# Performance work log

Hardware: AMD Instinct MI355X
Metric: run time of the kernel (lower is better)

Reference implementation:

```python
import jax, jax.numpy as jnp
import numpy as np

B, N, C, H = 1, 4096, 768, 12
HD = C // H  # 64
EPS = 1e-5


def _rope_freqs(n, hd, theta=10000.0):
    inv = 1.0 / (theta ** (np.arange(0, hd, 2, dtype=np.float32) / hd))  # (hd/2,)
    ang = np.outer(np.arange(n, dtype=np.float32), inv)  # (N, hd/2)
    return jnp.asarray(np.cos(ang)), jnp.asarray(np.sin(ang))


def setup_inputs() -> dict:
    key = jax.random.key(0)
    ks = jax.random.split(key, 5)
    cos, sin = _rope_freqs(N, HD)
    s = lambda d: 1.0 / np.sqrt(d)
    return {
        "x": jax.random.normal(ks[0], (B, N, C), jnp.float32),
        "freqs_cos": cos,
        "freqs_sin": sin,
        "w_qkv": jax.random.normal(ks[1], (3 * C, C), jnp.float32) * s(C),
        "w_proj": jax.random.normal(ks[2], (C, C), jnp.float32) * s(C),
        "b_proj": jnp.zeros((C,), jnp.float32),
        "g1": jnp.ones((C,), jnp.float32),
        "beta1": jnp.zeros((C,), jnp.float32),
        "g2": jnp.ones((C,), jnp.float32),
        "beta2": jnp.zeros((C,), jnp.float32),
        "w_fc1": jax.random.normal(ks[3], (4 * C, C), jnp.float32) * s(C),
        "b_fc1": jnp.zeros((4 * C,), jnp.float32),
        "w_fc2": jax.random.normal(ks[4], (C, 4 * C), jnp.float32) * s(4 * C),
        "b_fc2": jnp.zeros((C,), jnp.float32),
    }


def _layernorm(x, g, b):
    mu = jnp.mean(x, -1, keepdims=True)
    var = jnp.mean(jnp.square(x - mu), -1, keepdims=True)
    return (x - mu) * jax.lax.rsqrt(var + EPS) * g + b


def _apply_rope(t, cos, sin):
    # t: (B, N, H, HD); cos/sin: (N, HD/2) -> broadcast (1, N, 1, HD/2)
    t = t.reshape(*t.shape[:-1], HD // 2, 2)
    t0, t1 = t[..., 0], t[..., 1]
    c = cos[None, :, None, :]
    s = sin[None, :, None, :]
    out = jnp.stack([t0 * c - t1 * s, t0 * s + t1 * c], axis=-1)
    return out.reshape(*out.shape[:-2], HD)


def reference(x, freqs_cos, freqs_sin, w_qkv, w_proj, b_proj, g1, beta1, g2, beta2,
              w_fc1, b_fc1, w_fc2, b_fc2):
    # --- attention branch ---
    h = _layernorm(x, g1, beta1)
    qkv = (h @ w_qkv.T).reshape(B, N, 3, H, HD)
    q, k, v = qkv[:, :, 0], qkv[:, :, 1], qkv[:, :, 2]  # (B,N,H,HD)
    q = _apply_rope(q, freqs_cos, freqs_sin)
    k = _apply_rope(k, freqs_cos, freqs_sin)
    scale = HD ** (-0.5)
    attn = jnp.einsum('bnhd,bmhd->bhnm', q, k) * scale
    attn = jax.nn.softmax(attn, axis=-1)
    o = jnp.einsum('bhnm,bmhd->bnhd', attn, v).reshape(B, N, C)
    x = x + o @ w_proj.T + b_proj
    # --- mlp branch ---
    h = _layernorm(x, g2, beta2)
    h = jax.nn.gelu(h @ w_fc1.T + b_fc1, approximate=False)
    x = x + h @ w_fc2.T + b_fc2
    return x
```

## Files before the change

### kernel.cpp

```cpp
#include <hip/hip_runtime.h>
#include <hip/hip_bf16.h>
#include <math.h>

#define LOG2E 1.44269504088896340736f

typedef short bf16x8 __attribute__((ext_vector_type(8)));
typedef float f32x4 __attribute__((ext_vector_type(4)));

static __device__ __forceinline__ float bf2f(ushort u){
  union { float f; unsigned int u; } x; x.u = ((unsigned int)u) << 16; return x.f;
}
static __device__ __forceinline__ ushort f2bf(float f){
  union { float f; unsigned int u; } x; x.f = f;
  unsigned int r = x.u + 0x7fffu + ((x.u >> 16) & 1u);
  return (ushort)(r >> 16);
}
static __device__ __forceinline__ unsigned cvt_pk_bf16(float a, float b){
  unsigned r;
  asm("v_cvt_pk_bf16_f32 %0, %1, %2" : "=v"(r) : "v"(a), "v"(b));
  return r;
}
static __device__ __forceinline__ float fmax3(float a, float b, float c){
  return fmaxf(fmaxf(a, b), c);
}
static __device__ __forceinline__ void gload_lds16(const void* g, void* l){
  __builtin_amdgcn_global_load_lds(
      (const __attribute__((address_space(1))) unsigned int*)g,
      (__attribute__((address_space(3))) unsigned int*)l, 16, 0, 0);
}

__global__ __launch_bounds__(256) void cvt_f32_bf16(const float* __restrict__ src,
                                                    ushort* __restrict__ dst, int n4){
  int i = blockIdx.x * 256 + threadIdx.x;
  if (i < n4){
    float4 v = ((const float4*)src)[i];
    ushort4 o;
    o.x = f2bf(v.x); o.y = f2bf(v.y); o.z = f2bf(v.z); o.w = f2bf(v.w);
    ((ushort4*)dst)[i] = o;
  }
}

__device__ __forceinline__ float block_sum256(float s, float* red){
  #pragma unroll
  for (int off = 32; off; off >>= 1) s += __shfl_xor(s, off, 64);
  int w = threadIdx.x >> 6;
  if ((threadIdx.x & 63) == 0) red[w] = s;
  __syncthreads();
  float tot = red[0] + red[1] + red[2] + red[3];
  __syncthreads();
  return tot;
}

__global__ __launch_bounds__(256) void ln_kernel(const float* __restrict__ x,
                                                 const float* __restrict__ g,
                                                 const float* __restrict__ bta,
                                                 ushort* __restrict__ out){
  __shared__ float red[4];
  int row = blockIdx.x, t = threadIdx.x;
  const float* xr = x + (size_t)row * 768;
  float v0 = xr[t], v1 = xr[t + 256], v2 = xr[t + 512];
  float mu = block_sum256(v0 + v1 + v2, red) * (1.0f / 768.0f);
  float d0 = v0 - mu, d1 = v1 - mu, d2 = v2 - mu;
  float var = block_sum256(d0*d0 + d1*d1 + d2*d2, red) * (1.0f / 768.0f);
  float rs = rsqrtf(var + 1e-5f);
  ushort* orow = out + (size_t)row * 768;
  orow[t]       = f2bf(d0 * rs * g[t]       + bta[t]);
  orow[t + 256] = f2bf(d1 * rs * g[t + 256] + bta[t + 256]);
  orow[t + 512] = f2bf(d2 * rs * g[t + 512] + bta[t + 512]);
}

template<int MODE>
__global__ __launch_bounds__(256) void gemm_bf16(const ushort* __restrict__ A, int lda,
                                                 const ushort* __restrict__ Bm, int ldb,
                                                 int K,
                                                 const float* __restrict__ bias,
                                                 const float* __restrict__ res, int ldr,
                                                 void* __restrict__ out, int ldo){
  __shared__ __align__(16) ushort As[128 * 64];
  __shared__ __align__(16) ushort Bs[128 * 64];
  const int tid = threadIdx.x;
  const int m0 = blockIdx.x * 128, n0 = blockIdx.y * 128;
  const int w = tid >> 6, l = tid & 63;
  const int wm = (w >> 1) * 64, wn = (w & 1) * 64;
  const int lr = l & 15, lg = l >> 4;
  const int lane8 = l >> 3, sl = l & 7;
  const int koff = (MODE == 3) ? blockIdx.z * K : 0;

  f32x4 acc[4][4] = {};

  for (int k0 = 0; k0 < K; k0 += 64){
    #pragma unroll
    for (int j = 0; j < 4; ++j){
      int instr = w * 4 + j;
      int row = instr * 8 + lane8;
      gload_lds16((const char*)A + ((size_t)(m0 + row) * lda + koff + k0) * 2 + ((sl ^ (row & 7)) << 4),
                  (char*)As + instr * 1024);
      gload_lds16((const char*)Bm + ((size_t)(n0 + row) * ldb + koff + k0) * 2 + ((sl ^ (row & 7)) << 4),
                  (char*)Bs + instr * 1024);
    }
    __syncthreads();
    #pragma unroll
    for (int kk = 0; kk < 2; ++kk){
      bf16x8 af[4], bfr[4];
      #pragma unroll
      for (int mi = 0; mi < 4; ++mi){
        int row = wm + mi * 16 + lr;
        int cg = (kk * 4 + lg) ^ (row & 7);
        af[mi] = *(const bf16x8*)(As + row * 64 + cg * 8);
      }
      #pragma unroll
      for (int nj = 0; nj < 4; ++nj){
        int row = wn + nj * 16 + lr;
        int cg = (kk * 4 + lg) ^ (row & 7);
        bfr[nj] = *(const bf16x8*)(Bs + row * 64 + cg * 8);
      }
      #pragma unroll
      for (int mi = 0; mi < 4; ++mi)
        #pragma unroll
        for (int nj = 0; nj < 4; ++nj)
          acc[mi][nj] = __builtin_amdgcn_mfma_f32_16x16x32_bf16(af[mi], bfr[nj], acc[mi][nj], 0, 0, 0);
    }
    __syncthreads();
  }

  const size_t zout = (MODE == 3) ? (size_t)blockIdx.z * gridDim.x * 128 * ldo : 0;

  #pragma unroll
  for (int mi = 0; mi < 4; ++mi){
    #pragma unroll
    for (int nj = 0; nj < 4; ++nj){
      #pragma unroll
      for (int r = 0; r < 4; ++r){
        int grow = m0 + wm + mi * 16 + lg * 4 + r;
        int gcol = n0 + wn + nj * 16 + lr;
        float v = acc[mi][nj][r];
        if (MODE == 0){
          ((ushort*)out)[(size_t)grow * ldo + gcol] = f2bf(v);
        } else if (MODE == 1){
          v += bias[gcol] + res[(size_t)grow * ldr + gcol];
          ((float*)out)[(size_t)grow * ldo + gcol] = v;
        } else if (MODE == 2){
          v += bias[gcol];
          v = 0.5f * v * (1.0f + erff(v * 0.70710678118654752f));
          ((ushort*)out)[(size_t)grow * ldo + gcol] = f2bf(v);
        } else {
          ((float*)out)[zout + (size_t)grow * ldo + gcol] = v;
        }
      }
    }
  }
}

__global__ __launch_bounds__(192) void gemm_combine4(const float* __restrict__ parts,
                                                     const float* __restrict__ bias,
                                                     const float* __restrict__ res,
                                                     float* __restrict__ out){
  int q = blockIdx.x, t = threadIdx.x;
  size_t idx = (size_t)q * 768 + t * 4;
  const size_t seg = (size_t)4096 * 768;
  f32x4 o = *(const f32x4*)(parts + idx);
  #pragma unroll
  for (int s = 1; s < 4; ++s) o += *(const f32x4*)(parts + s * seg + idx);
  f32x4 b = *(const f32x4*)(bias + t * 4);
  f32x4 rr = *(const f32x4*)(res + idx);
  o += b + rr;
  *(f32x4*)(out + idx) = o;
}

__global__ __launch_bounds__(384) void rope_kernel(const ushort* __restrict__ qkv,
                                                   const float* __restrict__ fc,
                                                   const float* __restrict__ fs,
                                                   ushort* __restrict__ Qs,
                                                   ushort* __restrict__ Ks,
                                                   ushort* __restrict__ Vt){
  int n = blockIdx.x, t = threadIdx.x;
  int h = t >> 5, p = t & 31;
  float c = fc[(size_t)n * 32 + p], s = fs[(size_t)n * 32 + p];
  const ushort* row = qkv + (size_t)n * 2304;
  const float qscale = 0.125f * LOG2E;
  {
    float t0 = bf2f(row[h * 64 + 2 * p]), t1 = bf2f(row[h * 64 + 2 * p + 1]);
    ushort* dst = Qs + ((size_t)h * 4096 + n) * 64;
    dst[2 * p]     = f2bf((t0 * c - t1 * s) * qscale);
    dst[2 * p + 1] = f2bf((t0 * s + t1 * c) * qscale);
  }
  {
    float t0 = bf2f(row[768 + h * 64 + 2 * p]), t1 = bf2f(row[768 + h * 64 + 2 * p + 1]);
    ushort* dst = Ks + ((size_t)h * 4096 + n) * 64;
    dst[2 * p]     = f2bf(t0 * c - t1 * s);
    dst[2 * p + 1] = f2bf(t0 * s + t1 * c);
  }
  #pragma unroll
  for (int i = 0; i < 2; ++i){
    int idx = t + i * 384;
    int hh = idx >> 6, d = idx & 63;
    Vt[((size_t)hh * 64 + d) * 4096 + n] = row[1536 + idx];
  }
}

__global__ __launch_bounds__(256) void flash_attn(const ushort* __restrict__ Qs,
                                                  const ushort* __restrict__ Ks,
                                                  const ushort* __restrict__ Vt,
                                                  float* __restrict__ Opart,
                                                  float* __restrict__ Ml){
  __shared__ __align__(16) char smem[32768];
  const int h = blockIdx.y, kh = blockIdx.z;
  const int w = threadIdx.x >> 6, l = threadIdx.x & 63;
  const int lr = l & 15, lg = l >> 4;
  const int lane8 = l >> 3, sl = l & 7;
  const int q0 = blockIdx.x * 128 + w * 32;
  const ushort* Qh = Qs + (size_t)h * (4096 * 64);
  const char* Kh = (const char*)(Ks + (size_t)h * (4096 * 64));
  const char* Vh = (const char*)(Vt + (size_t)h * (64 * 4096));

  bf16x8 qa[2][2];
  #pragma unroll
  for (int qf = 0; qf < 2; ++qf)
    #pragma unroll
    for (int kk = 0; kk < 2; ++kk)
      qa[qf][kk] = *(const bf16x8*)(Qh + (size_t)(q0 + qf * 16 + lr) * 64 + kk * 32 + lg * 8);

  const char* kbase = Kh + (size_t)(kh * 1024 + w * 16 + lane8) * 128;
  const char* vbase = Vh + (size_t)(w * 16 + lane8) * 8192 + kh * 2048 + ((sl ^ lane8) << 4);
  int koff[2];
  #pragma unroll
  for (int j = 0; j < 2; ++j)
    koff[j] = j * 1024 + ((sl ^ ((lane8 & 3) | (((w * 2 + j) & 1) << 2))) << 4);

  const int a_ = lr >> 2, b_ = lr & 3;
  const int krow = 8 * a_ + b_;
  const int f_ = b_ | ((a_ & 1) << 2);
  const int kslot0 = (lg ^ f_) << 4;
  const int kslot1 = ((4 + lg) ^ f_) << 4;
  const int vslot0 = lr * 128 + ((lg ^ (lr & 7)) << 4);
  const int vslot1 = lr * 128 + (((4 + lg) ^ (lr & 7)) << 4);

  f32x4 oacc[2][4] = {};
  f32x4 lacc[2] = {};
  float m_prev[2] = {-1e30f, -1e30f};
  union { unsigned u[4]; bf16x8 v; } ones;
  #pragma unroll
  for (int i = 0; i < 4; ++i) ones.u[i] = 0x3F803F80u;

  auto stage = [&](int tile, char* Kb, char* Vb){
    #pragma unroll
    for (int j = 0; j < 2; ++j){
      gload_lds16(kbase + (size_t)tile * 8192 + koff[j], Kb + (w * 2 + j) * 1024);
      gload_lds16(vbase + (size_t)j * 65536 + (size_t)tile * 128, Vb + (w * 2 + j) * 1024);
    }
  };

  auto compute = [&](const char* Kb, const char* Vb){
    f32x4 s[2][4] = {};
    #pragma unroll
    for (int t = 0; t < 4; ++t){
      const char* kr = Kb + (krow + 4 * (t & 1) + 32 * (t >> 1)) * 128;
      bf16x8 k0 = *(const bf16x8*)(kr + kslot0);
      bf16x8 k1 = *(const bf16x8*)(kr + kslot1);
      #pragma unroll
      for (int qf = 0; qf < 2; ++qf){
        s[qf][t] = __builtin_amdgcn_mfma_f32_16x16x32_bf16(k0, qa[qf][0], s[qf][t], 0, 0, 0);
        s[qf][t] = __builtin_amdgcn_mfma_f32_16x16x32_bf16(k1, qa[qf][1], s[qf][t], 0, 0, 0);
      }
    }
    float mn[2];
    bool defer = true;
    #pragma unroll
    for (int qf = 0; qf < 2; ++qf){
      float m1 = fmax3(s[qf][0][0], s[qf][0][1], s[qf][0][2]);
      float m2 = fmax3(s[qf][0][3], s[qf][1][0], s[qf][1][1]);
      float m3 = fmax3(s[qf][1][2], s[qf][1][3], s[qf][2][0]);
      float m4 = fmax3(s[qf][2][1], s[qf][2][2], s[qf][2][3]);
      float m5 = fmax3(s[qf][3][0], s[qf][3][1], s[qf][3][2]);
      float mb = fmaxf(fmax3(m1, m2, m3), fmax3(m4, m5, s[qf][3][3]));
      mb = fmaxf(mb, __shfl_xor(mb, 16, 64));
      mb = fmaxf(mb, __shfl_xor(mb, 32, 64));
      bool d = (mb - m_prev[qf]) <= 8.0f;
      mn[qf] = d ? m_prev[qf] : mb;
      defer = defer && d;
    }
    if (!__all(defer)){
      #pragma unroll
      for (int qf = 0; qf < 2; ++qf){
        float sc = exp2f(m_prev[qf] - mn[qf]);
        #pragma unroll
        for (int db = 0; db < 4; ++db)
          #pragma unroll
          for (int r = 0; r < 4; ++r) oacc[qf][db][r] *= sc;
        #pragma unroll
        for (int r = 0; r < 4; ++r) lacc[qf][r] *= sc;
        m_prev[qf] = mn[qf];
      }
    }
    #pragma unroll
    for (int qf = 0; qf < 2; ++qf)
      #pragma unroll
      for (int t = 0; t < 4; ++t)
        #pragma unroll
        for (int r = 0; r < 4; ++r)
          s[qf][t][r] = exp2f(s[qf][t][r] - mn[qf]);
    #pragma unroll
    for (int kk = 0; kk < 2; ++kk){
      union { unsigned u[4]; bf16x8 v; } pf[2];
      #pragma unroll
      for (int qf = 0; qf < 2; ++qf){
        pf[qf].u[0] = cvt_pk_bf16(s[qf][2*kk][0],   s[qf][2*kk][1]);
        pf[qf].u[1] = cvt_pk_bf16(s[qf][2*kk][2],   s[qf][2*kk][3]);
        pf[qf].u[2] = cvt_pk_bf16(s[qf][2*kk+1][0], s[qf][2*kk+1][1]);
        pf[qf].u[3] = cvt_pk_bf16(s[qf][2*kk+1][2], s[qf][2*kk+1][3]);
      }
      const int vs = kk ? vslot1 : vslot0;
      #pragma unroll
      for (int db = 0; db < 4; ++db){
        bf16x8 vf = *(const bf16x8*)(Vb + vs + db * 2048);
        #pragma unroll
        for (int qf = 0; qf < 2; ++qf)
          oacc[qf][db] = __builtin_amdgcn_mfma_f32_16x16x32_bf16(vf, pf[qf].v, oacc[qf][db], 0, 0, 0);
      }
      #pragma unroll
      for (int qf = 0; qf < 2; ++qf)
        lacc[qf] = __builtin_amdgcn_mfma_f32_16x16x32_bf16(ones.v, pf[qf].v, lacc[qf], 0, 0, 0);
    }
  };

  char* K0 = smem;          char* V0 = smem + 8192;
  char* K1 = smem + 16384;  char* V1 = smem + 24576;

  stage(0, K0, V0);
  __syncthreads();
  #pragma unroll 1
  for (int it2 = 0; it2 < 8; ++it2){
    stage(2 * it2 + 1, K1, V1);
    compute(K0, V0);
    __syncthreads();
    if (it2 < 7) stage(2 * it2 + 2, K0, V0);
    compute(K1, V1);
    __syncthreads();
  }

  #pragma unroll
  for (int qf = 0; qf < 2; ++qf){
    int q = q0 + qf * 16 + lr;
    float* Op = Opart + ((size_t)(kh * 12 + h) * 4096 + q) * 64;
    #pragma unroll
    for (int db = 0; db < 4; ++db)
      *(f32x4*)(Op + db * 16 + 4 * lg) = oacc[qf][db];
    if (lg == 0){
      float2 ml; ml.x = m_prev[qf]; ml.y = lacc[qf][0];
      *(float2*)(Ml + ((size_t)(kh * 12 + h) * 4096 + q) * 2) = ml;
    }
  }
}

__global__ __launch_bounds__(192) void attn_combine(const float* __restrict__ Opart,
                                                    const float* __restrict__ Ml,
                                                    ushort* __restrict__ O){
  int q = blockIdx.x, t = threadIdx.x;
  int h = t >> 4;
  float2 ml[4];
  float m = -1e30f;
  #pragma unroll
  for (int s = 0; s < 4; ++s){
    ml[s] = *(const float2*)(Ml + ((size_t)(s * 12 + h) * 4096 + q) * 2);
    m = fmaxf(m, ml[s].x);
  }
  float wgt[4], lsum = 0.0f;
  #pragma unroll
  for (int s = 0; s < 4; ++s){
    wgt[s] = exp2f(ml[s].x - m);
    lsum += ml[s].y * wgt[s];
  }
  float inv = 1.0f / lsum;
  int dd = (t & 15) * 4;
  f32x4 o = {};
  #pragma unroll
  for (int s = 0; s < 4; ++s){
    f32x4 os = *(const f32x4*)(Opart + ((size_t)(s * 12 + h) * 4096 + q) * 64 + dd);
    #pragma unroll
    for (int r = 0; r < 4; ++r) o[r] += os[r] * wgt[s];
  }
  uint2 ov;
  ov.x = cvt_pk_bf16(o[0] * inv, o[1] * inv);
  ov.y = cvt_pk_bf16(o[2] * inv, o[3] * inv);
  *(uint2*)(O + (size_t)q * 768 + t * 4) = ov;
}

extern "C" void kernel_launch(void* const* d_in, const int* in_sizes, int n_in,
                              void* d_out, int out_size, void* d_ws, size_t ws_size,
                              hipStream_t stream){
  const float* x      = (const float*)d_in[0];
  const float* fcos   = (const float*)d_in[1];
  const float* fsin   = (const float*)d_in[2];
  const float* w_qkv  = (const float*)d_in[3];
  const float* w_proj = (const float*)d_in[4];
  const float* b_proj = (const float*)d_in[5];
  const float* g1     = (const float*)d_in[6];
  const float* beta1  = (const float*)d_in[7];
  const float* g2     = (const float*)d_in[8];
  const float* beta2  = (const float*)d_in[9];
  const float* w_fc1  = (const float*)d_in[10];
  const float* b_fc1  = (const float*)d_in[11];
  const float* w_fc2  = (const float*)d_in[12];
  const float* b_fc2  = (const float*)d_in[13];

  char* ws = (char*)d_ws;
  size_t off = 0;
  auto alloc = [&](size_t bytes) -> char* {
    char* p = ws + off; off += (bytes + 255) & ~(size_t)255; return p;
  };
  ushort* wq  = (ushort*)alloc((size_t)2304 * 768 * 2);
  ushort* wp  = (ushort*)alloc((size_t)768 * 768 * 2);
  ushort* w1  = (ushort*)alloc((size_t)3072 * 768 * 2);
  ushort* w2  = (ushort*)alloc((size_t)768 * 3072 * 2);
  ushort* h1  = (ushort*)alloc((size_t)4096 * 768 * 2);
  ushort* qkv = (ushort*)alloc((size_t)4096 * 2304 * 2);
  ushort* Qs  = (ushort*)alloc((size_t)12 * 4096 * 64 * 2);
  ushort* Ks  = (ushort*)alloc((size_t)12 * 4096 * 64 * 2);
  ushort* Vt  = (ushort*)alloc((size_t)12 * 64 * 4096 * 2);
  ushort* ao  = (ushort*)alloc((size_t)4096 * 768 * 2);
  float*  x2  = (float*) alloc((size_t)4096 * 768 * 4);
  ushort* h2  = (ushort*)alloc((size_t)4096 * 768 * 2);
  ushort* f1  = (ushort*)alloc((size_t)4096 * 3072 * 2);
  float*  Opart = (float*)alloc((size_t)4 * 12 * 4096 * 64 * 4);
  float*  Ml    = (float*)alloc((size_t)4 * 12 * 4096 * 2 * 4);
  float*  fc2p  = Opart;

  cvt_f32_bf16<<<(2304*768/4 + 255)/256, 256, 0, stream>>>(w_qkv,  wq, 2304*768/4);
  cvt_f32_bf16<<<(768*768/4  + 255)/256, 256, 0, stream>>>(w_proj, wp, 768*768/4);
  cvt_f32_bf16<<<(3072*768/4 + 255)/256, 256, 0, stream>>>(w_fc1,  w1, 3072*768/4);
  cvt_f32_bf16<<<(768*3072/4 + 255)/256, 256, 0, stream>>>(w_fc2,  w2, 768*3072/4);

  ln_kernel<<<4096, 256, 0, stream>>>(x, g1, beta1, h1);
  gemm_bf16<0><<<dim3(32, 18), 256, 0, stream>>>(h1, 768, wq, 768, 768,
                                                 nullptr, nullptr, 0, qkv, 2304);
  rope_kernel<<<4096, 384, 0, stream>>>(qkv, fcos, fsin, Qs, Ks, Vt);
  flash_attn<<<dim3(32, 12, 4), 256, 0, stream>>>(Qs, Ks, Vt, Opart, Ml);
  attn_combine<<<4096, 192, 0, stream>>>(Opart, Ml, ao);
  gemm_bf16<1><<<dim3(32, 6), 256, 0, stream>>>(ao, 768, wp, 768, 768,
                                                b_proj, x, 768, x2, 768);
  ln_kernel<<<4096, 256, 0, stream>>>(x2, g2, beta2, h2);
  gemm_bf16<2><<<dim3(32, 24), 256, 0, stream>>>(h2, 768, w1, 768, 768,
                                                 b_fc1, nullptr, 0, f1, 3072);
  gemm_bf16<3><<<dim3(32, 6, 4), 256, 0, stream>>>(f1, 3072, w2, 3072, 768,
                                                   nullptr, nullptr, 0, fc2p, 768);
  gemm_combine4<<<4096, 192, 0, stream>>>(fc2p, b_fc2, x2, (float*)d_out);
}
```

Before: 280.3 us.

## Split flash-attn softmax per half-tile, add occupancy hint, split-K the proj GEMM

The flash attention compute now handles each 32-key half of a tile on its own. The score accumulator is seeded with -m_prev, so the max subtraction comes out of the MFMA for free, and the running max is set from the first block instead of being updated lazily. This holds fewer live score registers, and a launch-bounds hint asks for 4 blocks per SM to raise occupancy. The projection GEMM moves to a 4-way split-K (K=192 per slice) with a separate combine kernel, which fills more CUs at the cost of an extra pass over fp32 partials.

```diff
diff --git a/kernel.cpp b/kernel.cpp
--- a/kernel.cpp
+++ b/kernel.cpp
@@ -198,11 +198,11 @@
   }
 }
 
-__global__ __launch_bounds__(256) void flash_attn(const ushort* __restrict__ Qs,
-                                                  const ushort* __restrict__ Ks,
-                                                  const ushort* __restrict__ Vt,
-                                                  float* __restrict__ Opart,
-                                                  float* __restrict__ Ml){
+__global__ __launch_bounds__(256, 4) void flash_attn(const ushort* __restrict__ Qs,
+                                                     const ushort* __restrict__ Ks,
+                                                     const ushort* __restrict__ Vt,
+                                                     float* __restrict__ Opart,
+                                                     float* __restrict__ Ml){
   __shared__ __align__(16) char smem[32768];
   const int h = blockIdx.y, kh = blockIdx.z;
   const int w = threadIdx.x >> 6, l = threadIdx.x & 63;
@@ -237,7 +237,7 @@
 
   f32x4 oacc[2][4] = {};
   f32x4 lacc[2] = {};
-  float m_prev[2] = {-1e30f, -1e30f};
+  float m_prev[2] = {0.0f, 0.0f};
   union { unsigned u[4]; bf16x8 v; } ones;
   #pragma unroll
   for (int i = 0; i < 4; ++i) ones.u[i] = 0x3F803F80u;
@@ -250,64 +250,82 @@
     }
   };
 
-  auto compute = [&](const char* Kb, const char* Vb){
-    f32x4 s[2][4] = {};
-    #pragma unroll
-    for (int t = 0; t < 4; ++t){
-      const char* kr = Kb + (krow + 4 * (t & 1) + 32 * (t >> 1)) * 128;
-      bf16x8 k0 = *(const bf16x8*)(kr + kslot0);
-      bf16x8 k1 = *(const bf16x8*)(kr + kslot1);
+  auto compute = [&](const char* Kb, const char* Vb, bool first){
+    #pragma unroll
+    for (int kk = 0; kk < 2; ++kk){
+      const bool fst = first && (kk == 0);
+      f32x4 sh[2][2];
       #pragma unroll
       for (int qf = 0; qf < 2; ++qf){
-        s[qf][t] = __builtin_amdgcn_mfma_f32_16x16x32_bf16(k0, qa[qf][0], s[qf][t], 0, 0, 0);
-        s[qf][t] = __builtin_amdgcn_mfma_f32_16x16x32_bf16(k1, qa[qf][1], s[qf][t], 0, 0, 0);
-      }
-    }
-    float mn[2];
-    bool defer = true;
-    #pragma unroll
-    for (int qf = 0; qf < 2; ++qf){
-      float m1 = fmax3(s[qf][0][0], s[qf][0][1], s[qf][0][2]);
-      float m2 = fmax3(s[qf][0][3], s[qf][1][0], s[qf][1][1]);
-      float m3 = fmax3(s[qf][1][2], s[qf][1][3], s[qf][2][0]);
-      float m4 = fmax3(s[qf][2][1], s[qf][2][2], s[qf][2][3]);
-      float m5 = fmax3(s[qf][3][0], s[qf][3][1], s[qf][3][2]);
-      float mb = fmaxf(fmax3(m1, m2, m3), fmax3(m4, m5, s[qf][3][3]));
-      mb = fmaxf(mb, __shfl_xor(mb, 16, 64));
-      mb = fmaxf(mb, __shfl_xor(mb, 32, 64));
-      bool d = (mb - m_prev[qf]) <= 8.0f;
-      mn[qf] = d ? m_prev[qf] : mb;
-      defer = defer && d;
-    }
-    if (!__all(defer)){
+        float iv = fst ? 0.0f : -m_prev[qf];
+        #pragma unroll
+        for (int tt = 0; tt < 2; ++tt){
+          sh[qf][tt][0] = iv; sh[qf][tt][1] = iv; sh[qf][tt][2] = iv; sh[qf][tt][3] = iv;
+        }
+      }
+      #pragma unroll
+      for (int tt = 0; tt < 2; ++tt){
+        const char* kr = Kb + (krow + 4 * tt + 32 * kk) * 128;
+        bf16x8 k0 = *(const bf16x8*)(kr + kslot0);
+        bf16x8 k1 = *(const bf16x8*)(kr + kslot1);
+        #pragma unroll
+        for (int qf = 0; qf < 2; ++qf){
+          sh[qf][tt] = __builtin_amdgcn_mfma_f32_16x16x32_bf16(k0, qa[qf][0], sh[qf][tt], 0, 0, 0);
+          sh[qf][tt] = __builtin_amdgcn_mfma_f32_16x16x32_bf16(k1, qa[qf][1], sh[qf][tt], 0, 0, 0);
+        }
+      }
+      float mb[2];
       #pragma unroll
       for (int qf = 0; qf < 2; ++qf){
-        float sc = exp2f(m_prev[qf] - mn[qf]);
-        #pragma unroll
-        for (int db = 0; db < 4; ++db)
+        float m1 = fmax3(sh[qf][0][0], sh[qf][0][1], sh[qf][0][2]);
+        float m2 = fmax3(sh[qf][0][3], sh[qf][1][0], sh[qf][1][1]);
+        float m3 = fmaxf(sh[qf][1][2], sh[qf][1][3]);
+        float mm = fmax3(m1, m2, m3);
+        mm = fmaxf(mm, __shfl_xor(mm, 16, 64));
+        mm = fmaxf(mm, __shfl_xor(mm, 32, 64));
+        mb[qf] = mm;
+      }
+      if (fst){
+        #pragma unroll
+        for (int qf = 0; qf < 2; ++qf){
+          m_prev[qf] = mb[qf];
           #pragma unroll
-          for (int r = 0; r < 4; ++r) oacc[qf][db][r] *= sc;
-        #pragma unroll
-        for (int r = 0; r < 4; ++r) lacc[qf][r] *= sc;
-        m_prev[qf] = mn[qf];
-      }
-    }
-    #pragma unroll
-    for (int qf = 0; qf < 2; ++qf)
-      #pragma unroll
-      for (int t = 0; t < 4; ++t)
-        #pragma unroll
-        for (int r = 0; r < 4; ++r)
-          s[qf][t][r] = exp2f(s[qf][t][r] - mn[qf]);
-    #pragma unroll
-    for (int kk = 0; kk < 2; ++kk){
+          for (int tt = 0; tt < 2; ++tt)
+            #pragma unroll
+            for (int r = 0; r < 4; ++r) sh[qf][tt][r] -= mb[qf];
+        }
+      } else if (!__all(mb[0] <= 8.0f && mb[1] <= 8.0f)){
+        #pragma unroll
+        for (int qf = 0; qf < 2; ++qf){
+          float d = (mb[qf] > 8.0f) ? mb[qf] : 0.0f;
+          float sc = exp2f(-d);
+          #pragma unroll
+          for (int tt = 0; tt < 2; ++tt)
+            #pragma unroll
+            for (int r = 0; r < 4; ++r) sh[qf][tt][r] -= d;
+          #pragma unroll
+          for (int db = 0; db < 4; ++db)
+            #pragma unroll
+            for (int r = 0; r < 4; ++r) oacc[qf][db][r] *= sc;
+          #pragma unroll
+          for (int r = 0; r < 4; ++r) lacc[qf][r] *= sc;
+          m_prev[qf] += d;
+        }
+      }
+      #pragma unroll
+      for (int qf = 0; qf < 2; ++qf)
+        #pragma unroll
+        for (int tt = 0; tt < 2; ++tt)
+          #pragma unroll
+          for (int r = 0; r < 4; ++r)
+            sh[qf][tt][r] = exp2f(sh[qf][tt][r]);
       union { unsigned u[4]; bf16x8 v; } pf[2];
       #pragma unroll
       for (int qf = 0; qf < 2; ++qf){
-        pf[qf].u[0] = cvt_pk_bf16(s[qf][2*kk][0],   s[qf][2*kk][1]);
-        pf[qf].u[1] = cvt_pk_bf16(s[qf][2*kk][2],   s[qf][2*kk][3]);
-        pf[qf].u[2] = cvt_pk_bf16(s[qf][2*kk+1][0], s[qf][2*kk+1][1]);
-        pf[qf].u[3] = cvt_pk_bf16(s[qf][2*kk+1][2], s[qf][2*kk+1][3]);
+        pf[qf].u[0] = cvt_pk_bf16(sh[qf][0][0], sh[qf][0][1]);
+        pf[qf].u[1] = cvt_pk_bf16(sh[qf][0][2], sh[qf][0][3]);
+        pf[qf].u[2] = cvt_pk_bf16(sh[qf][1][0], sh[qf][1][1]);
+        pf[qf].u[3] = cvt_pk_bf16(sh[qf][1][2], sh[qf][1][3]);
       }
       const int vs = kk ? vslot1 : vslot0;
       #pragma unroll
@@ -328,13 +346,19 @@
 
   stage(0, K0, V0);
   __syncthreads();
+  stage(1, K1, V1);
+  compute(K0, V0, true);
+  __syncthreads();
+  stage(2, K0, V0);
+  compute(K1, V1, false);
+  __syncthreads();
   #pragma unroll 1
-  for (int it2 = 0; it2 < 8; ++it2){
+  for (int it2 = 1; it2 < 8; ++it2){
     stage(2 * it2 + 1, K1, V1);
-    compute(K0, V0);
+    compute(K0, V0, false);
     __syncthreads();
     if (it2 < 7) stage(2 * it2 + 2, K0, V0);
-    compute(K1, V1);
+    compute(K1, V1, false);
     __syncthreads();
   }
 
@@ -423,7 +447,7 @@
   ushort* f1  = (ushort*)alloc((size_t)4096 * 3072 * 2);
   float*  Opart = (float*)alloc((size_t)4 * 12 * 4096 * 64 * 4);
   float*  Ml    = (float*)alloc((size_t)4 * 12 * 4096 * 2 * 4);
-  float*  fc2p  = Opart;
+  float*  skp   = Opart;
 
   cvt_f32_bf16<<<(2304*768/4 + 255)/256, 256, 0, stream>>>(w_qkv,  wq, 2304*768/4);
   cvt_f32_bf16<<<(768*768/4  + 255)/256, 256, 0, stream>>>(w_proj, wp, 768*768/4);
@@ -436,12 +460,13 @@
   rope_kernel<<<4096, 384, 0, stream>>>(qkv, fcos, fsin, Qs, Ks, Vt);
   flash_attn<<<dim3(32, 12, 4), 256, 0, stream>>>(Qs, Ks, Vt, Opart, Ml);
   attn_combine<<<4096, 192, 0, stream>>>(Opart, Ml, ao);
-  gemm_bf16<1><<<dim3(32, 6), 256, 0, stream>>>(ao, 768, wp, 768, 768,
-                                                b_proj, x, 768, x2, 768);
+  gemm_bf16<3><<<dim3(32, 6, 4), 256, 0, stream>>>(ao, 768, wp, 768, 192,
+                                                   nullptr, nullptr, 0, skp, 768);
+  gemm_combine4<<<4096, 192, 0, stream>>>(skp, b_proj, x, x2);
   ln_kernel<<<4096, 256, 0, stream>>>(x2, g2, beta2, h2);
   gemm_bf16<2><<<dim3(32, 24), 256, 0, stream>>>(h2, 768, w1, 768, 768,
                                                  b_fc1, nullptr, 0, f1, 3072);
   gemm_bf16<3><<<dim3(32, 6, 4), 256, 0, stream>>>(f1, 3072, w2, 3072, 768,
-                                                   nullptr, nullptr, 0, fc2p, 768);
-  gemm_combine4<<<4096, 192, 0, stream>>>(fc2p, b_fc2, x2, (float*)d_out);
-}
+                                                   nullptr, nullptr, 0, skp, 768);
+  gemm_combine4<<<4096, 192, 0, stream>>>(skp, b_fc2, x2, (float*)d_out);
+}
```

Result: no change. 278.9 us (-0.5%).
